# Optimization experiments

Hardware: AMD Instinct MI355X
Metric: run time of the kernel (lower is better)

Reference implementation:

```python
import jax, jax.numpy as jnp
import numpy as np

B, C, H, W, NH = 8, 192, 128, 128, 6  # batch, channels, height, width, heads


def setup_inputs() -> dict:
    key = jax.random.key(0)
    ks = jax.random.split(key, 5)
    return {
        "x": jax.random.normal(ks[0], (B, C, H, W), jnp.float32),
        "w_qkv": jax.random.normal(ks[1], (3 * C, 1, 3, 3), jnp.float32) * 0.1,  # grouped conv, groups=C
        "b_qkv": jax.random.normal(ks[2], (3 * C,), jnp.float32) * 0.1,
        "temperature": jnp.ones((NH, 1, 1), jnp.float32),
        "w_out": jax.random.normal(ks[3], (C, C), jnp.float32) * 0.05,  # 1x1 conv as dense
        "b_out": jax.random.normal(ks[4], (C,), jnp.float32) * 0.05,
    }


def reference(x, w_qkv, b_qkv, temperature, w_out, b_out):
    b, c, h, w = x.shape
    nh = temperature.shape[0]
    # grouped 3x3 conv (groups = in_ch), padding=1
    qkv = jax.lax.conv_general_dilated(
        x, w_qkv, window_strides=(1, 1), padding=[(1, 1), (1, 1)],
        feature_group_count=c, dimension_numbers=("NCHW", "OIHW", "NCHW"),
    ) + b_qkv[None, :, None, None]
    q, k, v = jnp.split(qkv, 3, axis=1)  # each [b, c, h, w]

    def to_heads(t):
        return t.reshape(b, nh, c // nh, h * w)  # b head c (h w)

    q, k, v = to_heads(q), to_heads(k), to_heads(v)
    eps = 1e-12  # F.normalize default
    q = q / jnp.maximum(jnp.linalg.norm(q, axis=-1, keepdims=True), eps)
    k = k / jnp.maximum(jnp.linalg.norm(k, axis=-1, keepdims=True), eps)
    attn = jnp.einsum("bhcn,bhdn->bhcd", q, k) * temperature[None]  # [b, nh, c/nh, c/nh]
    attn = jax.nn.softmax(attn, axis=-1)
    out = jnp.einsum("bhcd,bhdn->bhcn", attn, v).reshape(b, c, h, w)
    out = jnp.einsum("oc,bchw->bohw", w_out, out) + b_out[None, :, None, None]
    return out
```

## Files before the change

kernel.cpp:

```cpp
#include <hip/hip_runtime.h>
#include <hip/hip_bf16.h>

constexpr int B   = 8;
constexpr int Cc  = 192;
constexpr int H   = 128;
constexpr int Wd  = 128;
constexpr int NH  = 6;
constexpr int HW  = H * Wd;
constexpr int QKV = 3 * Cc;

typedef short s16x8 __attribute__((ext_vector_type(8)));
typedef float f32x16 __attribute__((ext_vector_type(16)));

constexpr size_t OFF_QKV  = 0;
constexpr size_t OFF_ATTN = 150994944ULL;
constexpr size_t OFF_SSQ  = OFF_ATTN + 196608ULL;
constexpr size_t OFF_M    = OFF_SSQ + 12288ULL;
constexpr int    N_ZERO   = (196608 + 12288) / 4;

__device__ inline unsigned short f2bf(float f) {
    __hip_bfloat16 h = __float2bfloat16(f);
    return *(unsigned short*)&h;
}

__global__ void zero_kernel(float* __restrict__ p, int n) {
    int i = blockIdx.x * 256 + threadIdx.x;
    if (i < n) p[i] = 0.f;
}

constexpr int TS = 16;

__global__ __launch_bounds__(256) void conv_qkv(
    const float* __restrict__ x, const float* __restrict__ w,
    const float* __restrict__ bias, unsigned short* __restrict__ qkv,
    float* __restrict__ ssq)
{
    int tile = blockIdx.x;
    int g    = blockIdx.y;
    int b    = blockIdx.z;
    int y0   = tile * TS;

    __shared__ float sm[TS + 2][132];
    __shared__ float red[256];

    const float* xp = x + ((size_t)b * Cc + g) * HW;
    for (int i = threadIdx.x; i < (TS + 2) * 32; i += 256) {
        int r = i >> 5, c4 = (i & 31) * 4;
        int y = y0 - 1 + r;
        if (y >= 0 && y < H) {
            float4 v4 = *(const float4*)(xp + (size_t)y * Wd + c4);
            sm[r][c4 + 1] = v4.x; sm[r][c4 + 2] = v4.y;
            sm[r][c4 + 3] = v4.z; sm[r][c4 + 4] = v4.w;
        } else {
            sm[r][c4 + 1] = 0.f; sm[r][c4 + 2] = 0.f;
            sm[r][c4 + 3] = 0.f; sm[r][c4 + 4] = 0.f;
        }
    }
    for (int i = threadIdx.x; i < (TS + 2) * 2; i += 256) {
        int r = i >> 1;
        sm[r][(i & 1) ? 129 : 0] = 0.f;
    }
    __syncthreads();

    float wreg[3][9], breg[3];
    for (int j = 0; j < 3; ++j) {
        const float* wp = w + (size_t)(3 * g + j) * 9;
        for (int t = 0; t < 9; ++t) wreg[j][t] = wp[t];
        breg[j] = bias[3 * g + j];
    }

    bool track = (g < 128);
    float ss[3] = {0.f, 0.f, 0.f};

    int xq = (threadIdx.x & 31) * 4;
    int ys = threadIdx.x >> 5;

    for (int yy = ys; yy < TS; yy += 8) {
        float rv[3][6];
        for (int r = 0; r < 3; ++r) {
            float4 a4 = *(const float4*)&sm[yy + r][xq];
            float2 a2 = *(const float2*)&sm[yy + r][xq + 4];
            rv[r][0] = a4.x; rv[r][1] = a4.y; rv[r][2] = a4.z;
            rv[r][3] = a4.w; rv[r][4] = a2.x; rv[r][5] = a2.y;
        }
        for (int j = 0; j < 3; ++j) {
            unsigned short pk[4];
            for (int xx = 0; xx < 4; ++xx) {
                float s = breg[j]
                    + wreg[j][0] * rv[0][xx] + wreg[j][1] * rv[0][xx + 1] + wreg[j][2] * rv[0][xx + 2]
                    + wreg[j][3] * rv[1][xx] + wreg[j][4] * rv[1][xx + 1] + wreg[j][5] * rv[1][xx + 2]
                    + wreg[j][6] * rv[2][xx] + wreg[j][7] * rv[2][xx + 1] + wreg[j][8] * rv[2][xx + 2];
                if (track) ss[j] += s * s;
                pk[xx] = f2bf(s);
            }
            unsigned short* op = qkv + ((size_t)b * QKV + 3 * g + j) * HW
                                     + (size_t)(y0 + yy) * Wd + xq;
            *(ushort4*)op = make_ushort4(pk[0], pk[1], pk[2], pk[3]);
        }
    }

    if (track) {
        for (int j = 0; j < 3; ++j) {
            red[threadIdx.x] = ss[j];
            __syncthreads();
            for (int st = 128; st > 0; st >>= 1) {
                if (threadIdx.x < st) red[threadIdx.x] += red[threadIdx.x + st];
                __syncthreads();
            }
            if (threadIdx.x == 0) {
                int o = 3 * g + j;
                atomicAdd(&ssq[(o < Cc ? 0 : 1) * B * Cc + b * Cc + (o % Cc)], red[0]);
            }
            __syncthreads();
        }
    }
}

constexpr int NSEG = 64;
constexpr int SEGN = HW / NSEG;

__global__ __launch_bounds__(256) void qk_mfma(
    const unsigned short* __restrict__ qkv, float* __restrict__ attn)
{
    int h = blockIdx.y, b = blockIdx.z;
    int tid = threadIdx.x;
    int wv = tid >> 6, lane = tid & 63;
    int seg = blockIdx.x * 4 + wv;
    int col = lane & 31, half = lane >> 5;

    __shared__ float sacc[1024];
    for (int i = tid; i < 1024; i += 256) sacc[i] = 0.f;
    __syncthreads();

    const unsigned short* qp = qkv + ((size_t)b * QKV + h * 32 + col) * HW
                                   + seg * SEGN + half * 8;
    const unsigned short* kp = qp + (size_t)Cc * HW;

    f32x16 acc0, acc1;
    for (int i = 0; i < 16; ++i) { acc0[i] = 0.f; acc1[i] = 0.f; }

    for (int kk = 0; kk < SEGN; kk += 32) {
        s16x8 a0 = *(const s16x8*)(qp + kk);
        s16x8 b0 = *(const s16x8*)(kp + kk);
        acc0 = __builtin_amdgcn_mfma_f32_32x32x16_bf16(a0, b0, acc0, 0, 0, 0);
        s16x8 a1 = *(const s16x8*)(qp + kk + 16);
        s16x8 b1 = *(const s16x8*)(kp + kk + 16);
        acc1 = __builtin_amdgcn_mfma_f32_32x32x16_bf16(a1, b1, acc1, 0, 0, 0);
    }

    int rb = half * 4;
    for (int r = 0; r < 16; ++r) {
        int row = (r & 3) + 8 * (r >> 2) + rb;
        atomicAdd(&sacc[row * 32 + col], acc0[r] + acc1[r]);
    }
    __syncthreads();
    float* ap = attn + (size_t)(b * NH + h) * 1024;
    for (int i = tid; i < 1024; i += 256) atomicAdd(&ap[i], sacc[i]);
}

__global__ void softmax_attn(float* __restrict__ attn,
                             const float* __restrict__ ssq,
                             const float* __restrict__ temp)
{
    int h = blockIdx.x % NH, b = blockIdx.x / NH;
    __shared__ float nk[32];
    if (threadIdx.x < 32)
        nk[threadIdx.x] = fmaxf(sqrtf(ssq[B * Cc + b * Cc + h * 32 + threadIdx.x]), 1e-12f);
    __syncthreads();
    int c = threadIdx.x;
    if (c >= 32) return;
    float nq = fmaxf(sqrtf(ssq[b * Cc + h * 32 + c]), 1e-12f);
    float t = temp[h];
    float* ap = attn + ((size_t)(b * NH + h) * 32 + c) * 32;
    float row[32];
    float mx = -1e30f;
    for (int d = 0; d < 32; ++d) {
        float v = ap[d] / (nq * nk[d]) * t;
        row[d] = v;
        mx = fmaxf(mx, v);
    }
    float sum = 0.f;
    for (int d = 0; d < 32; ++d) { row[d] = expf(row[d] - mx); sum += row[d]; }
    float inv = 1.f / sum;
    for (int d = 0; d < 32; ++d) ap[d] = row[d] * inv;
}

__global__ __launch_bounds__(256) void make_m(
    const float* __restrict__ attn, const float* __restrict__ w_out,
    unsigned short* __restrict__ M)
{
    int h = blockIdx.x, b = blockIdx.y;
    __shared__ float as[32][33];
    for (int i = threadIdx.x; i < 1024; i += 256)
        as[i / 32][i % 32] = attn[(size_t)((b * NH + h) * 32 + i / 32) * 32 + i % 32];
    __syncthreads();
    for (int i = threadIdx.x; i < Cc * 32; i += 256) {
        int o = i / 32, d = i % 32;
        const float* wp = w_out + (size_t)o * Cc + h * 32;
        float s = 0.f;
        for (int cp = 0; cp < 32; ++cp) s += wp[cp] * as[cp][d];
        M[((size_t)b * Cc + o) * Cc + h * 32 + d] = f2bf(s);
    }
}

constexpr int BN = 128;

__global__ __launch_bounds__(256) void out_gemm(
    const unsigned short* __restrict__ M, const unsigned short* __restrict__ qkv,
    const float* __restrict__ b_out, float* __restrict__ out)
{
    int n0 = blockIdx.x * BN;
    int b  = blockIdx.y;

    const unsigned short* vp = qkv + ((size_t)b * QKV + 2 * Cc) * HW;
    const unsigned short* mp = M + (size_t)b * Cc * Cc;

    __shared__ unsigned short vsT[BN][24];

    int tid  = threadIdx.x;
    int lane = tid & 63, wv = tid >> 6;
    int wm = wv & 1, wn = wv >> 1;
    int col = lane & 31, half = lane >> 5;

    f32x16 acc[6];
    for (int t = 0; t < 6; ++t)
        for (int i = 0; i < 16; ++i) acc[t][i] = 0.f;

    int p  = tid >> 5;
    int nq = tid & 31;

    for (int k0 = 0; k0 < Cc; k0 += 16) {
        const unsigned short* s0 = vp + (size_t)(k0 + 2 * p) * HW + n0 + 4 * nq;
        ushort4 va = *(const ushort4*)s0;
        ushort4 vb = *(const ushort4*)(s0 + HW);
        *(unsigned int*)&vsT[4 * nq + 0][2 * p] = (unsigned int)va.x | ((unsigned int)vb.x << 16);
        *(unsigned int*)&vsT[4 * nq + 1][2 * p] = (unsigned int)va.y | ((unsigned int)vb.y << 16);
        *(unsigned int*)&vsT[4 * nq + 2][2 * p] = (unsigned int)va.z | ((unsigned int)vb.z << 16);
        *(unsigned int*)&vsT[4 * nq + 3][2 * p] = (unsigned int)va.w | ((unsigned int)vb.w << 16);
        __syncthreads();

        s16x8 af[3], bf[2];
        for (int mt = 0; mt < 3; ++mt) {
            int o = wm * 96 + mt * 32 + col;
            af[mt] = *(const s16x8*)(mp + (size_t)o * Cc + k0 + half * 8);
        }
        for (int nt = 0; nt < 2; ++nt) {
            int nn = wn * 64 + nt * 32 + col;
            bf[nt] = *(const s16x8*)&vsT[nn][half * 8];
        }
        for (int mt = 0; mt < 3; ++mt)
            for (int nt = 0; nt < 2; ++nt)
                acc[mt * 2 + nt] = __builtin_amdgcn_mfma_f32_32x32x16_bf16(
                    af[mt], bf[nt], acc[mt * 2 + nt], 0, 0, 0);
        __syncthreads();
    }

    for (int mt = 0; mt < 3; ++mt)
        for (int nt = 0; nt < 2; ++nt) {
            f32x16 c = acc[mt * 2 + nt];
            int n = n0 + wn * 64 + nt * 32 + col;
            for (int r = 0; r < 16; ++r) {
                int row = (r & 3) + 8 * (r >> 2) + 4 * half;
                int o = wm * 96 + mt * 32 + row;
                out[((size_t)b * Cc + o) * HW + n] = c[r] + b_out[o];
            }
        }
}

extern "C" void kernel_launch(void* const* d_in, const int* in_sizes, int n_in,
                              void* d_out, int out_size, void* d_ws, size_t ws_size,
                              hipStream_t stream) {
    const float* x      = (const float*)d_in[0];
    const float* w_qkv  = (const float*)d_in[1];
    const float* b_qkv  = (const float*)d_in[2];
    const float* temp   = (const float*)d_in[3];
    const float* w_out  = (const float*)d_in[4];
    const float* b_out  = (const float*)d_in[5];
    float* out = (float*)d_out;

    char* ws = (char*)d_ws;
    unsigned short* qkv = (unsigned short*)(ws + OFF_QKV);
    float* attn         = (float*)(ws + OFF_ATTN);
    float* ssq          = (float*)(ws + OFF_SSQ);
    unsigned short* M   = (unsigned short*)(ws + OFF_M);

    zero_kernel<<<(N_ZERO + 255) / 256, 256, 0, stream>>>(attn, N_ZERO);
    conv_qkv<<<dim3(H / TS, Cc, B), 256, 0, stream>>>(x, w_qkv, b_qkv, qkv, ssq);
    qk_mfma<<<dim3(NSEG / 4, NH, B), 256, 0, stream>>>(qkv, attn);
    softmax_attn<<<B * NH, 64, 0, stream>>>(attn, ssq, temp);
    make_m<<<dim3(NH, B), 256, 0, stream>>>(attn, w_out, M);
    out_gemm<<<dim3(HW / BN, B), 256, 0, stream>>>(M, qkv, b_out, out);
}
```

Before: 285.1 us.

## Fuse depthwise QKV conv with QK^T MFMA, keep Q/K in LDS

Merges the grouped 3x3 conv and the Q·K^T MFMA into one kernel. Q and K strips are written as bf16 into shared memory and consumed there, so only V goes to global memory. This removes the write and re-read of the Q and K tensors (two thirds of the bf16 qkv buffer) and one launch. In exchange each thread reads x rows straight from global memory with halo reloads instead of staging them in shared memory. The grid shrinks to H/8 x NH x B blocks, which may lower parallelism for the conv work.

```diff
diff --git a/kernel.cpp b/kernel.cpp
--- a/kernel.cpp
+++ b/kernel.cpp
@@ -6,14 +6,14 @@
 constexpr int H   = 128;
 constexpr int Wd  = 128;
 constexpr int NH  = 6;
+constexpr int HD  = 32;
 constexpr int HW  = H * Wd;
-constexpr int QKV = 3 * Cc;
 
 typedef short s16x8 __attribute__((ext_vector_type(8)));
 typedef float f32x16 __attribute__((ext_vector_type(16)));
 
-constexpr size_t OFF_QKV  = 0;
-constexpr size_t OFF_ATTN = 150994944ULL;
+constexpr size_t OFF_V    = 0;
+constexpr size_t OFF_ATTN = 50331648ULL;
 constexpr size_t OFF_SSQ  = OFF_ATTN + 196608ULL;
 constexpr size_t OFF_M    = OFF_SSQ + 12288ULL;
 constexpr int    N_ZERO   = (196608 + 12288) / 4;
@@ -28,134 +28,130 @@
     if (i < n) p[i] = 0.f;
 }
 
-constexpr int TS = 16;
-
-__global__ __launch_bounds__(256) void conv_qkv(
+__device__ __forceinline__ void ldrow(const float* __restrict__ xg, int yr,
+                                      int xl, float (&r)[6]) {
+    if (yr >= 0 && yr < H) {
+        const float* p = xg + (size_t)yr * Wd + xl;
+        float4 m = *(const float4*)p;
+        r[0] = (xl > 0) ? p[-1] : 0.f;
+        r[1] = m.x; r[2] = m.y; r[3] = m.z; r[4] = m.w;
+        r[5] = (xl + 4 < Wd) ? p[4] : 0.f;
+    } else {
+        r[0] = 0.f; r[1] = 0.f; r[2] = 0.f; r[3] = 0.f; r[4] = 0.f; r[5] = 0.f;
+    }
+}
+
+template<bool TO_LDS>
+__device__ __forceinline__ float conv_strip(
+    const float* __restrict__ xg, const float (&wr)[9], float br,
+    int y0, int xl, unsigned short* __restrict__ ldsp,
+    int q8, int ch, unsigned short* __restrict__ gp)
+{
+    float rv[3][6];
+    ldrow(xg, y0 - 1, xl, rv[0]);
+    ldrow(xg, y0,     xl, rv[1]);
+    float ss = 0.f;
+#pragma unroll
+    for (int y = 0; y < 8; ++y) {
+        ldrow(xg, y0 + y + 1, xl, rv[(y + 2) % 3]);
+        const float* r0 = rv[y % 3];
+        const float* r1 = rv[(y + 1) % 3];
+        const float* r2 = rv[(y + 2) % 3];
+        float o[4];
+#pragma unroll
+        for (int xx = 0; xx < 4; ++xx) {
+            o[xx] = br
+                + wr[0] * r0[xx] + wr[1] * r0[xx + 1] + wr[2] * r0[xx + 2]
+                + wr[3] * r1[xx] + wr[4] * r1[xx + 1] + wr[5] * r1[xx + 2]
+                + wr[6] * r2[xx] + wr[7] * r2[xx + 1] + wr[8] * r2[xx + 2];
+        }
+        ss += o[0] * o[0] + o[1] * o[1] + o[2] * o[2] + o[3] * o[3];
+        ushort4 pk = make_ushort4(f2bf(o[0]), f2bf(o[1]), f2bf(o[2]), f2bf(o[3]));
+        if (TO_LDS) {
+            int g = 4 * y + (q8 >> 1);
+            *(ushort4*)(ldsp + ((g * 32 + ch) << 3) + ((q8 & 1) << 2)) = pk;
+        } else {
+            *(ushort4*)(gp + (size_t)(y0 + y) * Wd) = pk;
+        }
+    }
+    return ss;
+}
+
+__global__ __launch_bounds__(256) void fused_conv_qk(
     const float* __restrict__ x, const float* __restrict__ w,
-    const float* __restrict__ bias, unsigned short* __restrict__ qkv,
-    float* __restrict__ ssq)
-{
-    int tile = blockIdx.x;
-    int g    = blockIdx.y;
-    int b    = blockIdx.z;
-    int y0   = tile * TS;
-
-    __shared__ float sm[TS + 2][132];
-    __shared__ float red[256];
-
-    const float* xp = x + ((size_t)b * Cc + g) * HW;
-    for (int i = threadIdx.x; i < (TS + 2) * 32; i += 256) {
-        int r = i >> 5, c4 = (i & 31) * 4;
-        int y = y0 - 1 + r;
-        if (y >= 0 && y < H) {
-            float4 v4 = *(const float4*)(xp + (size_t)y * Wd + c4);
-            sm[r][c4 + 1] = v4.x; sm[r][c4 + 2] = v4.y;
-            sm[r][c4 + 3] = v4.z; sm[r][c4 + 4] = v4.w;
-        } else {
-            sm[r][c4 + 1] = 0.f; sm[r][c4 + 2] = 0.f;
-            sm[r][c4 + 3] = 0.f; sm[r][c4 + 4] = 0.f;
-        }
-    }
-    for (int i = threadIdx.x; i < (TS + 2) * 2; i += 256) {
-        int r = i >> 1;
-        sm[r][(i & 1) ? 129 : 0] = 0.f;
-    }
-    __syncthreads();
-
-    float wreg[3][9], breg[3];
-    for (int j = 0; j < 3; ++j) {
-        const float* wp = w + (size_t)(3 * g + j) * 9;
-        for (int t = 0; t < 9; ++t) wreg[j][t] = wp[t];
-        breg[j] = bias[3 * g + j];
-    }
-
-    bool track = (g < 128);
-    float ss[3] = {0.f, 0.f, 0.f};
-
-    int xq = (threadIdx.x & 31) * 4;
-    int ys = threadIdx.x >> 5;
-
-    for (int yy = ys; yy < TS; yy += 8) {
-        float rv[3][6];
-        for (int r = 0; r < 3; ++r) {
-            float4 a4 = *(const float4*)&sm[yy + r][xq];
-            float2 a2 = *(const float2*)&sm[yy + r][xq + 4];
-            rv[r][0] = a4.x; rv[r][1] = a4.y; rv[r][2] = a4.z;
-            rv[r][3] = a4.w; rv[r][4] = a2.x; rv[r][5] = a2.y;
-        }
-        for (int j = 0; j < 3; ++j) {
-            unsigned short pk[4];
-            for (int xx = 0; xx < 4; ++xx) {
-                float s = breg[j]
-                    + wreg[j][0] * rv[0][xx] + wreg[j][1] * rv[0][xx + 1] + wreg[j][2] * rv[0][xx + 2]
-                    + wreg[j][3] * rv[1][xx] + wreg[j][4] * rv[1][xx + 1] + wreg[j][5] * rv[1][xx + 2]
-                    + wreg[j][6] * rv[2][xx] + wreg[j][7] * rv[2][xx + 1] + wreg[j][8] * rv[2][xx + 2];
-                if (track) ss[j] += s * s;
-                pk[xx] = f2bf(s);
-            }
-            unsigned short* op = qkv + ((size_t)b * QKV + 3 * g + j) * HW
-                                     + (size_t)(y0 + yy) * Wd + xq;
-            *(ushort4*)op = make_ushort4(pk[0], pk[1], pk[2], pk[3]);
-        }
-    }
-
-    if (track) {
-        for (int j = 0; j < 3; ++j) {
-            red[threadIdx.x] = ss[j];
-            __syncthreads();
-            for (int st = 128; st > 0; st >>= 1) {
-                if (threadIdx.x < st) red[threadIdx.x] += red[threadIdx.x + st];
-                __syncthreads();
-            }
-            if (threadIdx.x == 0) {
-                int o = 3 * g + j;
-                atomicAdd(&ssq[(o < Cc ? 0 : 1) * B * Cc + b * Cc + (o % Cc)], red[0]);
-            }
-            __syncthreads();
-        }
-    }
-}
-
-constexpr int NSEG = 64;
-constexpr int SEGN = HW / NSEG;
-
-__global__ __launch_bounds__(256) void qk_mfma(
-    const unsigned short* __restrict__ qkv, float* __restrict__ attn)
-{
-    int h = blockIdx.y, b = blockIdx.z;
-    int tid = threadIdx.x;
-    int wv = tid >> 6, lane = tid & 63;
-    int seg = blockIdx.x * 4 + wv;
-    int col = lane & 31, half = lane >> 5;
-
-    __shared__ float sacc[1024];
+    const float* __restrict__ bias, unsigned short* __restrict__ vws,
+    float* __restrict__ ssq, float* __restrict__ attn)
+{
+    const int tile = blockIdx.x, h = blockIdx.y, b = blockIdx.z;
+    const int y0  = tile * 8;
+    const int tid = threadIdx.x;
+    const int ch  = tid >> 3, q8 = tid & 7;
+    const int lane = tid & 63, wv = tid >> 6;
+
+    __shared__ unsigned short qs[32 * 32 * 8];
+    __shared__ unsigned short ks[32 * 32 * 8];
+
+    const int oc = h * HD + ch;
+    const float* xq = x + ((size_t)b * Cc + oc / 3) * HW;
+    const float* xk = x + ((size_t)b * Cc + (Cc + oc) / 3) * HW;
+    const float* xv = x + ((size_t)b * Cc + (2 * Cc + oc) / 3) * HW;
+
+    float wq[9], wk[9], wvv[9];
+#pragma unroll
+    for (int t = 0; t < 9; ++t) {
+        wq[t]  = w[(size_t)oc * 9 + t];
+        wk[t]  = w[(size_t)(Cc + oc) * 9 + t];
+        wvv[t] = w[(size_t)(2 * Cc + oc) * 9 + t];
+    }
+    const float bq = bias[oc], bk = bias[Cc + oc], bv = bias[2 * Cc + oc];
+
+    unsigned short* vout = vws + ((size_t)b * Cc + oc) * HW;
+
+    f32x16 acc;
+#pragma unroll
+    for (int i = 0; i < 16; ++i) acc[i] = 0.f;
+    float ssq_a = 0.f, ssk_a = 0.f;
+
+    const int m = lane & 31, hf = lane >> 5;
+
+#pragma unroll 1
+    for (int s = 0; s < 4; ++s) {
+        const int xl = s * 32 + 4 * q8;
+        __syncthreads();
+        ssq_a += conv_strip<true >(xq, wq,  bq, y0, xl, qs, q8, ch, nullptr);
+        ssk_a += conv_strip<true >(xk, wk,  bk, y0, xl, ks, q8, ch, nullptr);
+        conv_strip<false>(xv, wvv, bv, y0, xl, nullptr, q8, ch, vout + xl);
+        __syncthreads();
+#pragma unroll
+        for (int cc = 0; cc < 4; ++cc) {
+            int g = (wv * 4 + cc) * 2 + hf;
+            s16x8 qa = *(const s16x8*)&qs[(g * 32 + m) << 3];
+            s16x8 kb = *(const s16x8*)&ks[(g * 32 + m) << 3];
+            acc = __builtin_amdgcn_mfma_f32_32x32x16_bf16(qa, kb, acc, 0, 0, 0);
+        }
+    }
+
+    __syncthreads();
+    float* sacc = (float*)qs;
     for (int i = tid; i < 1024; i += 256) sacc[i] = 0.f;
     __syncthreads();
-
-    const unsigned short* qp = qkv + ((size_t)b * QKV + h * 32 + col) * HW
-                                   + seg * SEGN + half * 8;
-    const unsigned short* kp = qp + (size_t)Cc * HW;
-
-    f32x16 acc0, acc1;
-    for (int i = 0; i < 16; ++i) { acc0[i] = 0.f; acc1[i] = 0.f; }
-
-    for (int kk = 0; kk < SEGN; kk += 32) {
-        s16x8 a0 = *(const s16x8*)(qp + kk);
-        s16x8 b0 = *(const s16x8*)(kp + kk);
-        acc0 = __builtin_amdgcn_mfma_f32_32x32x16_bf16(a0, b0, acc0, 0, 0, 0);
-        s16x8 a1 = *(const s16x8*)(qp + kk + 16);
-        s16x8 b1 = *(const s16x8*)(kp + kk + 16);
-        acc1 = __builtin_amdgcn_mfma_f32_32x32x16_bf16(a1, b1, acc1, 0, 0, 0);
-    }
-
-    int rb = half * 4;
+#pragma unroll
     for (int r = 0; r < 16; ++r) {
-        int row = (r & 3) + 8 * (r >> 2) + rb;
-        atomicAdd(&sacc[row * 32 + col], acc0[r] + acc1[r]);
+        int row = (r & 3) + 8 * (r >> 2) + 4 * hf;
+        atomicAdd(&sacc[row * 32 + m], acc[r]);
     }
     __syncthreads();
     float* ap = attn + (size_t)(b * NH + h) * 1024;
     for (int i = tid; i < 1024; i += 256) atomicAdd(&ap[i], sacc[i]);
+
+    for (int off = 4; off; off >>= 1) {
+        ssq_a += __shfl_down(ssq_a, off, 8);
+        ssk_a += __shfl_down(ssk_a, off, 8);
+    }
+    if (q8 == 0) {
+        atomicAdd(&ssq[b * Cc + oc], ssq_a);
+        atomicAdd(&ssq[B * Cc + b * Cc + oc], ssk_a);
+    }
 }
 
 __global__ void softmax_attn(float* __restrict__ attn,
@@ -206,13 +202,13 @@
 constexpr int BN = 128;
 
 __global__ __launch_bounds__(256) void out_gemm(
-    const unsigned short* __restrict__ M, const unsigned short* __restrict__ qkv,
+    const unsigned short* __restrict__ vws, const unsigned short* __restrict__ M,
     const float* __restrict__ b_out, float* __restrict__ out)
 {
     int n0 = blockIdx.x * BN;
     int b  = blockIdx.y;
 
-    const unsigned short* vp = qkv + ((size_t)b * QKV + 2 * Cc) * HW;
+    const unsigned short* vp = vws + (size_t)b * Cc * HW;
     const unsigned short* mp = M + (size_t)b * Cc * Cc;
 
     __shared__ unsigned short vsT[BN][24];
@@ -279,15 +275,14 @@
     float* out = (float*)d_out;
 
     char* ws = (char*)d_ws;
-    unsigned short* qkv = (unsigned short*)(ws + OFF_QKV);
+    unsigned short* vws = (unsigned short*)(ws + OFF_V);
     float* attn         = (float*)(ws + OFF_ATTN);
     float* ssq          = (float*)(ws + OFF_SSQ);
     unsigned short* M   = (unsigned short*)(ws + OFF_M);
 
     zero_kernel<<<(N_ZERO + 255) / 256, 256, 0, stream>>>(attn, N_ZERO);
-    conv_qkv<<<dim3(H / TS, Cc, B), 256, 0, stream>>>(x, w_qkv, b_qkv, qkv, ssq);
-    qk_mfma<<<dim3(NSEG / 4, NH, B), 256, 0, stream>>>(qkv, attn);
+    fused_conv_qk<<<dim3(H / 8, NH, B), 256, 0, stream>>>(x, w_qkv, b_qkv, vws, ssq, attn);
     softmax_attn<<<B * NH, 64, 0, stream>>>(attn, ssq, temp);
     make_m<<<dim3(NH, B), 256, 0, stream>>>(attn, w_out, M);
-    out_gemm<<<dim3(HW / BN, B), 256, 0, stream>>>(M, qkv, b_out, out);
-}
+    out_gemm<<<dim3(HW / BN, B), 256, 0, stream>>>(vws, M, b_out, out);
+}
```

Measured after the change: 427.3 us. 49.9% more time.
